# Performance work log

Hardware: AMD Instinct MI355X
Metric: run time of the kernel (lower is better)

The kernel has to match this reference:

```python
import jax, jax.numpy as jnp
import numpy as np

NUM_EXPERTS = 256
TOP_K = 8
N_GROUP = 8
TOPK_GROUP = 4
ROUTED_SCALING_FACTOR = 2.5


def setup_inputs() -> dict:
    key = jax.random.key(0)
    k1, k2, k3 = jax.random.split(key, 3)
    B, H, E = 16384, 7168, NUM_EXPERTS
    hidden_states = jax.random.normal(k1, (B, H), dtype=jnp.float32)
    weight = jax.random.normal(k2, (E, H), dtype=jnp.float32) * 0.02
    e_score_correction_bias = jax.random.normal(k3, (E,), dtype=jnp.float32) * 0.01
    return {
        "hidden_states": hidden_states,
        "weight": weight,
        "e_score_correction_bias": e_score_correction_bias,
    }


def reference(hidden_states, weight, e_score_correction_bias):
    B = hidden_states.shape[0]
    experts_per_group = NUM_EXPERTS // N_GROUP
    # router logits: [B, E] (small skinny GEMM)
    router_logits = jnp.einsum("bh,eh->be", hidden_states.astype(jnp.float32), weight.astype(jnp.float32))
    # torch casts to f64 for sigmoid then back; f32 sigmoid is numerically equivalent here
    scores = jax.nn.sigmoid(router_logits).astype(hidden_states.dtype)
    scores_for_choice = scores + e_score_correction_bias[None, :]
    # per-group score = sum of top-2 expert scores in the group
    grp = scores_for_choice.reshape(B, N_GROUP, experts_per_group)
    top2_vals, _ = jax.lax.top_k(grp, 2)          # [B, G, 2]
    group_scores = top2_vals.sum(axis=-1)          # [B, G]
    # pick topk_group groups, build group mask via scatter
    _, group_idx = jax.lax.top_k(group_scores, TOPK_GROUP)  # [B, topk_group]
    group_mask = jnp.zeros((B, N_GROUP), dtype=scores_for_choice.dtype)
    group_mask = group_mask.at[jnp.arange(B)[:, None], group_idx].set(1.0)
    # expand group mask to experts and mask scores
    score_mask = jnp.broadcast_to(group_mask[:, :, None], (B, N_GROUP, experts_per_group)).reshape(B, -1)
    masked_scores = jnp.where(score_mask > 0, scores_for_choice, 0.0)
    # final expert top-k on masked (bias-corrected) scores
    _, topk_indices = jax.lax.top_k(masked_scores, TOP_K)   # [B, top_k]
    # weights gathered from the UN-biased sigmoid scores, then normalize + scale
    topk_weights = jnp.take_along_axis(scores, topk_indices, axis=1)
    topk_weights = topk_weights / topk_weights.sum(axis=-1, keepdims=True)
    topk_weights = topk_weights * ROUTED_SCALING_FACTOR
    return topk_indices, topk_weights
```

## Files before the change

### kernel.cpp

```cpp
#include <hip/hip_runtime.h>
#include <math.h>

#define B_ROWS 16384
#define H_DIM 7168
#define N_EXP 256
#define KT 32
#define MT 64
#define ET 128

__global__ __launch_bounds__(256, 2)
void router_gemm_f64(const float* __restrict__ hs, const float* __restrict__ w,
                     float* __restrict__ scores) {
    __shared__ double As[KT][MT + 2];
    __shared__ double Ws[4][KT][34];
    const int t = threadIdx.x;
    const int tx = t & 15;
    const int ty = t >> 4;
    const int mBase = blockIdx.x * MT;
    const int eBase = blockIdx.y * ET;
    const float* hsp = hs + (size_t)mBase * H_DIM;
    const float* wp  = w  + (size_t)eBase * H_DIM;

    double acc[4][8];
#pragma unroll
    for (int r = 0; r < 4; ++r)
#pragma unroll
        for (int c = 0; c < 8; ++c) acc[r][c] = 0.0;

    float4 ha[2], wa[4];
#pragma unroll
    for (int i = 0; i < 2; ++i) {
        int flat = i * 1024 + t * 4;
        ha[i] = *(const float4*)(hsp + (size_t)(flat >> 5) * H_DIM + (flat & 31));
    }
#pragma unroll
    for (int i = 0; i < 4; ++i) {
        int flat = i * 1024 + t * 4;
        wa[i] = *(const float4*)(wp + (size_t)(flat >> 5) * H_DIM + (flat & 31));
    }

    const int NCHUNK = H_DIM / KT;
    for (int ch = 0; ch < NCHUNK; ++ch) {
        {
            const int row = (t >> 3);
            const int kk  = 4 * (t & 7);
#pragma unroll
            for (int i = 0; i < 2; ++i) {
                const int rr = i * 32 + row;
                As[kk + 0][rr] = (double)ha[i].x;
                As[kk + 1][rr] = (double)ha[i].y;
                As[kk + 2][rr] = (double)ha[i].z;
                As[kk + 3][rr] = (double)ha[i].w;
            }
#pragma unroll
            for (int i = 0; i < 4; ++i) {
                Ws[i][kk + 0][row] = (double)wa[i].x;
                Ws[i][kk + 1][row] = (double)wa[i].y;
                Ws[i][kk + 2][row] = (double)wa[i].z;
                Ws[i][kk + 3][row] = (double)wa[i].w;
            }
        }
        __syncthreads();
        if (ch + 1 < NCHUNK) {
            const float* hp2 = hsp + (size_t)(ch + 1) * KT;
            const float* wp2 = wp  + (size_t)(ch + 1) * KT;
#pragma unroll
            for (int i = 0; i < 2; ++i) {
                int flat = i * 1024 + t * 4;
                ha[i] = *(const float4*)(hp2 + (size_t)(flat >> 5) * H_DIM + (flat & 31));
            }
#pragma unroll
            for (int i = 0; i < 4; ++i) {
                int flat = i * 1024 + t * 4;
                wa[i] = *(const float4*)(wp2 + (size_t)(flat >> 5) * H_DIM + (flat & 31));
            }
        }
#pragma unroll
        for (int k = 0; k < KT; ++k) {
            double2 a0 = *(const double2*)&As[k][ty * 4];
            double2 a1 = *(const double2*)&As[k][ty * 4 + 2];
            double2 b0 = *(const double2*)&Ws[0][k][tx * 2];
            double2 b1 = *(const double2*)&Ws[1][k][tx * 2];
            double2 b2 = *(const double2*)&Ws[2][k][tx * 2];
            double2 b3 = *(const double2*)&Ws[3][k][tx * 2];
            double a_[4] = {a0.x, a0.y, a1.x, a1.y};
            double b_[8] = {b0.x, b0.y, b1.x, b1.y, b2.x, b2.y, b3.x, b3.y};
#pragma unroll
            for (int r = 0; r < 4; ++r)
#pragma unroll
                for (int c = 0; c < 8; ++c)
                    acc[r][c] = fma(a_[r], b_[c], acc[r][c]);
        }
        __syncthreads();
    }
#pragma unroll
    for (int r = 0; r < 4; ++r) {
        const int row = mBase + ty * 4 + r;
        float* dst = scores + (size_t)row * N_EXP + eBase;
#pragma unroll
        for (int q = 0; q < 4; ++q) {
            double s0 = 1.0 / (1.0 + exp(-acc[r][2 * q + 0]));
            double s1 = 1.0 / (1.0 + exp(-acc[r][2 * q + 1]));
            *(float2*)(dst + q * 32 + tx * 2) = make_float2((float)s0, (float)s1);
        }
    }
}

__global__ __launch_bounds__(256)
void router_topk_kernel(const float* __restrict__ scores, const float* __restrict__ bias,
                        float* __restrict__ out) {
    const int lane = threadIdx.x & 63;
    const int row = (blockIdx.x * blockDim.x + threadIdx.x) >> 6;

    float4 s4 = *(const float4*)(scores + (size_t)row * N_EXP + lane * 4);
    float4 b4 = *(const float4*)(bias + lane * 4);
    float sc[4]  = {s4.x, s4.y, s4.z, s4.w};
    float sfc[4] = {sc[0] + b4.x, sc[1] + b4.y, sc[2] + b4.z, sc[3] + b4.w};

    float m1 = -1e30f, m2 = -1e30f;
#pragma unroll
    for (int i = 0; i < 4; ++i) {
        float v = sfc[i];
        if (v > m1) { m2 = m1; m1 = v; }
        else if (v > m2) m2 = v;
    }
#pragma unroll
    for (int off = 1; off <= 4; off <<= 1) {
        float o1 = __shfl_xor(m1, off);
        float o2 = __shfl_xor(m2, off);
        float n1 = fmaxf(m1, o1);
        float n2 = fmaxf(fminf(m1, o1), fmaxf(m2, o2));
        m1 = n1; m2 = n2;
    }
    float gs = m1 + m2;
    int g = lane >> 3;
    int rank = 0;
#pragma unroll
    for (int j = 0; j < 8; ++j) {
        float gj = __shfl(gs, j * 8);
        rank += (gj > gs || (gj == gs && j < g)) ? 1 : 0;
    }
    bool sel = rank < 4;
    float mv[4];
#pragma unroll
    for (int i = 0; i < 4; ++i) mv[i] = sel ? sfc[i] : 0.0f;

    float wsum = 0.f;
    float myIdxF = 0.f, myW = 0.f;
    for (int it = 0; it < 8; ++it) {
        float bv = mv[0]; int bi = 0;
#pragma unroll
        for (int i = 1; i < 4; ++i)
            if (mv[i] > bv) { bv = mv[i]; bi = i; }
        int bidx = lane * 4 + bi;
        float bsc = sc[bi];
#pragma unroll
        for (int off = 1; off <= 32; off <<= 1) {
            float ov = __shfl_xor(bv, off);
            int   oi = __shfl_xor(bidx, off);
            float os = __shfl_xor(bsc, off);
            if (ov > bv || (ov == bv && oi < bidx)) { bv = ov; bidx = oi; bsc = os; }
        }
        wsum += bsc;
        if (lane == it) { myIdxF = (float)bidx; myW = bsc; }
        if ((bidx >> 2) == lane) mv[bidx & 3] = -1e30f;
    }
    if (lane < 8) {
        out[(size_t)row * 8 + lane] = myIdxF;
        out[(size_t)B_ROWS * 8 + (size_t)row * 8 + lane] = myW * (2.5f / wsum);
    }
}

extern "C" void kernel_launch(void* const* d_in, const int* in_sizes, int n_in,
                              void* d_out, int out_size, void* d_ws, size_t ws_size,
                              hipStream_t stream) {
    const float* hs   = (const float*)d_in[0];
    const float* w    = (const float*)d_in[1];
    const float* bias = (const float*)d_in[2];
    float* out = (float*)d_out;
    float* scores = (float*)d_ws;

    dim3 g1(B_ROWS / MT, N_EXP / ET);
    router_gemm_f64<<<g1, 256, 0, stream>>>(hs, w, scores);
    router_topk_kernel<<<B_ROWS / 4, 256, 0, stream>>>(scores, bias, out);
}
```

Measured before the change: 1.870 ms.

## Use FP64 MFMA for router GEMM with runtime layout self-check fallback

```diff
diff --git a/kernel.cpp b/kernel.cpp
--- a/kernel.cpp
+++ b/kernel.cpp
@@ -8,100 +8,189 @@
 #define MT 64
 #define ET 128
 
+using v4d = __attribute__((ext_vector_type(4))) double;
+
 __global__ __launch_bounds__(256, 2)
-void router_gemm_f64(const float* __restrict__ hs, const float* __restrict__ w,
-                     float* __restrict__ scores) {
-    __shared__ double As[KT][MT + 2];
-    __shared__ double Ws[4][KT][34];
+void router_gemm(const float* __restrict__ hs, const float* __restrict__ w,
+                 float* __restrict__ scores) {
+    __shared__ float AfU[2304];
+    __shared__ float WfU[4608];
+    __shared__ int okSh;
+
     const int t = threadIdx.x;
+    const int lane = t & 63;
+    const int wv = t >> 6;
+    const int fm = lane & 15;
+    const int kg = lane >> 4;
     const int tx = t & 15;
     const int ty = t >> 4;
+    const int row8 = t >> 3;
+    const int kq8 = t & 7;
+
     const int mBase = blockIdx.x * MT;
     const int eBase = blockIdx.y * ET;
     const float* hsp = hs + (size_t)mBase * H_DIM;
     const float* wp  = w  + (size_t)eBase * H_DIM;
 
-    double acc[4][8];
+    bool ok = true;
+#pragma unroll 1
+    for (int p = 0; p < 3; ++p) {
+        for (int i = t; i < 64 * 36; i += 256) {
+            int m = i / 36, kk = i % 36;
+            int k = (kk & 7) * 4 + (kk >> 3);
+            AfU[i] = (p == 0) ? (float)(4 * m + k + 1)
+                   : (p == 2) ? (float)(k + 1) : 1.0f;
+        }
+        for (int i = t; i < 128 * 36; i += 256) {
+            int e = i / 36, kk = i % 36;
+            int k = (kk & 7) * 4 + (kk >> 3);
+            WfU[i] = (p == 1) ? (float)(4 * e + k + 1)
+                   : (p == 2) ? (float)(k + 1) : 1.0f;
+        }
+        __syncthreads();
+        double a = (double)AfU[fm * 36 + 8 * kg];
+        double b = (double)WfU[fm * 36 + 8 * kg];
+        v4d z = {0.0, 0.0, 0.0, 0.0};
+        v4d pr = __builtin_amdgcn_mfma_f64_16x16x4f64(a, b, z, 0, 0, 0);
+#pragma unroll
+        for (int r = 0; r < 4; ++r) {
+            double ev = (p == 0) ? (double)(16 * (4 * kg + r) + 10)
+                      : (p == 1) ? (double)(16 * fm + 10) : 30.0;
+            ok = ok && (pr[r] == ev);
+        }
+        __syncthreads();
+    }
+    if (t == 0) okSh = 1;
+    __syncthreads();
+    if (!ok) okSh = 0;
+    __syncthreads();
+    const bool useMfma = (okSh != 0);
+
+    union AccU { double v[4][8]; v4d m[4][2]; } acc;
 #pragma unroll
     for (int r = 0; r < 4; ++r)
 #pragma unroll
-        for (int c = 0; c < 8; ++c) acc[r][c] = 0.0;
-
-    float4 ha[2], wa[4];
-#pragma unroll
-    for (int i = 0; i < 2; ++i) {
-        int flat = i * 1024 + t * 4;
-        ha[i] = *(const float4*)(hsp + (size_t)(flat >> 5) * H_DIM + (flat & 31));
-    }
-#pragma unroll
-    for (int i = 0; i < 4; ++i) {
-        int flat = i * 1024 + t * 4;
-        wa[i] = *(const float4*)(wp + (size_t)(flat >> 5) * H_DIM + (flat & 31));
-    }
+        for (int c = 0; c < 8; ++c) acc.v[r][c] = 0.0;
+
+    float haf[2][4], waf[4][4];
+#pragma unroll
+    for (int i = 0; i < 2; ++i)
+        *(float4*)&haf[i][0] = *(const float4*)(hsp + (size_t)(i * 32 + row8) * H_DIM + 4 * kq8);
+#pragma unroll
+    for (int i = 0; i < 4; ++i)
+        *(float4*)&waf[i][0] = *(const float4*)(wp + (size_t)(i * 32 + row8) * H_DIM + 4 * kq8);
 
     const int NCHUNK = H_DIM / KT;
     for (int ch = 0; ch < NCHUNK; ++ch) {
-        {
-            const int row = (t >> 3);
-            const int kk  = 4 * (t & 7);
-#pragma unroll
-            for (int i = 0; i < 2; ++i) {
-                const int rr = i * 32 + row;
-                As[kk + 0][rr] = (double)ha[i].x;
-                As[kk + 1][rr] = (double)ha[i].y;
-                As[kk + 2][rr] = (double)ha[i].z;
-                As[kk + 3][rr] = (double)ha[i].w;
-            }
-#pragma unroll
-            for (int i = 0; i < 4; ++i) {
-                Ws[i][kk + 0][row] = (double)wa[i].x;
-                Ws[i][kk + 1][row] = (double)wa[i].y;
-                Ws[i][kk + 2][row] = (double)wa[i].z;
-                Ws[i][kk + 3][row] = (double)wa[i].w;
-            }
+        if (useMfma) {
+#pragma unroll
+            for (int i = 0; i < 2; ++i)
+#pragma unroll
+                for (int j = 0; j < 4; ++j)
+                    AfU[(i * 32 + row8) * 36 + 8 * j + kq8] = haf[i][j];
+#pragma unroll
+            for (int i = 0; i < 4; ++i)
+#pragma unroll
+                for (int j = 0; j < 4; ++j)
+                    WfU[(i * 32 + row8) * 36 + 8 * j + kq8] = waf[i][j];
+        } else {
+#pragma unroll
+            for (int i = 0; i < 2; ++i)
+#pragma unroll
+                for (int j = 0; j < 4; ++j)
+                    AfU[(4 * kq8 + j) * 68 + i * 32 + row8] = haf[i][j];
+#pragma unroll
+            for (int i = 0; i < 4; ++i)
+#pragma unroll
+                for (int j = 0; j < 4; ++j)
+                    WfU[(4 * kq8 + j) * 132 + i * 32 + row8] = waf[i][j];
         }
         __syncthreads();
         if (ch + 1 < NCHUNK) {
             const float* hp2 = hsp + (size_t)(ch + 1) * KT;
             const float* wp2 = wp  + (size_t)(ch + 1) * KT;
 #pragma unroll
-            for (int i = 0; i < 2; ++i) {
-                int flat = i * 1024 + t * 4;
-                ha[i] = *(const float4*)(hp2 + (size_t)(flat >> 5) * H_DIM + (flat & 31));
-            }
-#pragma unroll
-            for (int i = 0; i < 4; ++i) {
-                int flat = i * 1024 + t * 4;
-                wa[i] = *(const float4*)(wp2 + (size_t)(flat >> 5) * H_DIM + (flat & 31));
-            }
-        }
-#pragma unroll
-        for (int k = 0; k < KT; ++k) {
-            double2 a0 = *(const double2*)&As[k][ty * 4];
-            double2 a1 = *(const double2*)&As[k][ty * 4 + 2];
-            double2 b0 = *(const double2*)&Ws[0][k][tx * 2];
-            double2 b1 = *(const double2*)&Ws[1][k][tx * 2];
-            double2 b2 = *(const double2*)&Ws[2][k][tx * 2];
-            double2 b3 = *(const double2*)&Ws[3][k][tx * 2];
-            double a_[4] = {a0.x, a0.y, a1.x, a1.y};
-            double b_[8] = {b0.x, b0.y, b1.x, b1.y, b2.x, b2.y, b3.x, b3.y};
-#pragma unroll
-            for (int r = 0; r < 4; ++r)
-#pragma unroll
-                for (int c = 0; c < 8; ++c)
-                    acc[r][c] = fma(a_[r], b_[c], acc[r][c]);
-        }
-        __syncthreads();
-    }
-#pragma unroll
-    for (int r = 0; r < 4; ++r) {
-        const int row = mBase + ty * 4 + r;
-        float* dst = scores + (size_t)row * N_EXP + eBase;
-#pragma unroll
-        for (int q = 0; q < 4; ++q) {
-            double s0 = 1.0 / (1.0 + exp(-acc[r][2 * q + 0]));
-            double s1 = 1.0 / (1.0 + exp(-acc[r][2 * q + 1]));
-            *(float2*)(dst + q * 32 + tx * 2) = make_float2((float)s0, (float)s1);
+            for (int i = 0; i < 2; ++i)
+                *(float4*)&haf[i][0] = *(const float4*)(hp2 + (size_t)(i * 32 + row8) * H_DIM + 4 * kq8);
+#pragma unroll
+            for (int i = 0; i < 4; ++i)
+                *(float4*)&waf[i][0] = *(const float4*)(wp2 + (size_t)(i * 32 + row8) * H_DIM + 4 * kq8);
+        }
+        if (useMfma) {
+            float afr[4][8], bfr[2][8];
+#pragma unroll
+            for (int rs = 0; rs < 4; ++rs) {
+                const int base = (rs * 16 + fm) * 36 + 8 * kg;
+                *(float4*)&afr[rs][0] = *(float4*)&AfU[base];
+                *(float4*)&afr[rs][4] = *(float4*)&AfU[base + 4];
+            }
+#pragma unroll
+            for (int cs = 0; cs < 2; ++cs) {
+                const int base = (wv * 32 + cs * 16 + fm) * 36 + 8 * kg;
+                *(float4*)&bfr[cs][0] = *(float4*)&WfU[base];
+                *(float4*)&bfr[cs][4] = *(float4*)&WfU[base + 4];
+            }
+#pragma unroll
+            for (int q = 0; q < 8; ++q) {
+                double aq0 = (double)afr[0][q], aq1 = (double)afr[1][q];
+                double aq2 = (double)afr[2][q], aq3 = (double)afr[3][q];
+                double bq0 = (double)bfr[0][q], bq1 = (double)bfr[1][q];
+                acc.m[0][0] = __builtin_amdgcn_mfma_f64_16x16x4f64(aq0, bq0, acc.m[0][0], 0, 0, 0);
+                acc.m[0][1] = __builtin_amdgcn_mfma_f64_16x16x4f64(aq0, bq1, acc.m[0][1], 0, 0, 0);
+                acc.m[1][0] = __builtin_amdgcn_mfma_f64_16x16x4f64(aq1, bq0, acc.m[1][0], 0, 0, 0);
+                acc.m[1][1] = __builtin_amdgcn_mfma_f64_16x16x4f64(aq1, bq1, acc.m[1][1], 0, 0, 0);
+                acc.m[2][0] = __builtin_amdgcn_mfma_f64_16x16x4f64(aq2, bq0, acc.m[2][0], 0, 0, 0);
+                acc.m[2][1] = __builtin_amdgcn_mfma_f64_16x16x4f64(aq2, bq1, acc.m[2][1], 0, 0, 0);
+                acc.m[3][0] = __builtin_amdgcn_mfma_f64_16x16x4f64(aq3, bq0, acc.m[3][0], 0, 0, 0);
+                acc.m[3][1] = __builtin_amdgcn_mfma_f64_16x16x4f64(aq3, bq1, acc.m[3][1], 0, 0, 0);
+            }
+        } else {
+#pragma unroll
+            for (int k = 0; k < KT; ++k) {
+                float4 af  = *(float4*)&AfU[k * 68 + ty * 4];
+                float4 bfa = *(float4*)&WfU[k * 132 + tx * 4];
+                float4 bfb = *(float4*)&WfU[k * 132 + 64 + tx * 4];
+                double a_[4] = {(double)af.x, (double)af.y, (double)af.z, (double)af.w};
+                double b_[8] = {(double)bfa.x, (double)bfa.y, (double)bfa.z, (double)bfa.w,
+                                (double)bfb.x, (double)bfb.y, (double)bfb.z, (double)bfb.w};
+#pragma unroll
+                for (int r = 0; r < 4; ++r)
+#pragma unroll
+                    for (int c = 0; c < 8; ++c)
+                        acc.v[r][c] = fma(a_[r], b_[c], acc.v[r][c]);
+            }
+        }
+        __syncthreads();
+    }
+
+    if (useMfma) {
+#pragma unroll
+        for (int rs = 0; rs < 4; ++rs)
+#pragma unroll
+            for (int cs = 0; cs < 2; ++cs)
+#pragma unroll
+                for (int r = 0; r < 4; ++r) {
+                    const int rr = mBase + rs * 16 + 4 * kg + r;
+                    const int cc = eBase + wv * 32 + cs * 16 + fm;
+                    double s = 1.0 / (1.0 + exp(-acc.m[rs][cs][r]));
+                    scores[(size_t)rr * N_EXP + cc] = (float)s;
+                }
+    } else {
+#pragma unroll
+        for (int r = 0; r < 4; ++r) {
+            const int rr = mBase + ty * 4 + r;
+            float* dst = scores + (size_t)rr * N_EXP + eBase;
+            float4 o0, o1;
+            o0.x = (float)(1.0 / (1.0 + exp(-acc.v[r][0])));
+            o0.y = (float)(1.0 / (1.0 + exp(-acc.v[r][1])));
+            o0.z = (float)(1.0 / (1.0 + exp(-acc.v[r][2])));
+            o0.w = (float)(1.0 / (1.0 + exp(-acc.v[r][3])));
+            o1.x = (float)(1.0 / (1.0 + exp(-acc.v[r][4])));
+            o1.y = (float)(1.0 / (1.0 + exp(-acc.v[r][5])));
+            o1.z = (float)(1.0 / (1.0 + exp(-acc.v[r][6])));
+            o1.w = (float)(1.0 / (1.0 + exp(-acc.v[r][7])));
+            *(float4*)(dst + tx * 4) = o0;
+            *(float4*)(dst + 64 + tx * 4) = o1;
         }
     }
 }
@@ -181,6 +270,6 @@
     float* scores = (float*)d_ws;
 
     dim3 g1(B_ROWS / MT, N_EXP / ET);
-    router_gemm_f64<<<g1, 256, 0, stream>>>(hs, w, scores);
+    router_gemm<<<g1, 256, 0, stream>>>(hs, w, scores);
     router_topk_kernel<<<B_ROWS / 4, 256, 0, stream>>>(scores, bias, out);
 }
```

Measured after the change: 1.986 ms. 1.06x slower.
